# Performance work log

Measured on AMD Instinct MI355X. Metric: run time of the kernel, lower is better.

The kernel has to match this reference:

```python
import jax, jax.numpy as jnp
import numpy as np

B, S, D, H = 4, 2048, 1024, 16
DH = D // H


def setup_inputs() -> dict:
    key = jax.random.key(0)
    k1, k2, k3, k4, k5 = jax.random.split(key, 5)
    X = jax.random.normal(k1, (B, S, D), dtype=jnp.float32)
    W1 = jax.random.normal(k2, (3 * D, D), dtype=jnp.float32) * 0.02
    b1 = jax.random.normal(k3, (3 * D,), dtype=jnp.float32) * 0.01
    W2 = jax.random.normal(k4, (D, D), dtype=jnp.float32) * 0.02
    b2 = jax.random.normal(k5, (D,), dtype=jnp.float32) * 0.01
    return {"X": X, "W1": W1, "b1": b1, "W2": W2, "b2": b2}


def reference(X, W1, b1, W2, b2):
    b, s, d = X.shape
    # fused QKV projection (nn.Linear: y = x @ W.T + b)
    Y = X @ W1.T + b1                                   # [B,S,3D]
    Q, K, V = jnp.split(Y, 3, axis=2)                   # each [B,S,D]
    # reshape(x): view (B,S,H,DH) then permute(0,2,3,1) -> [B,H,DH,S]
    q = Q.reshape(b, s, H, DH).transpose(0, 2, 3, 1)    # [B,H,DH,S]
    v = V.reshape(b, s, H, DH).transpose(0, 2, 3, 1)    # [B,H,DH,S]
    # reshape(x, k=True): permute(0,2,1,3) -> [B,H,S,DH]
    k = K.reshape(b, s, H, DH).transpose(0, 2, 1, 3)    # [B,H,S,DH]
    # w = q @ k / sqrt(q.size(-1)) ; note q.size(-1) == S in this layout
    w = jnp.einsum('bhds,bhse->bhde', q, k) / jnp.sqrt(jnp.asarray(s, X.dtype))  # [B,H,DH,DH]
    w = jax.nn.softmax(w, axis=-1)
    out = jnp.einsum('bhde,bhes->bhds', w, v)           # [B,H,DH,S]
    # cat(): raw contiguous view of [B,H,DH,S] into [B,S,H*DH] (memory-order reshape)
    out = out.reshape(b, s, H * DH)                     # [B,S,D]
    return out @ W2.T + b2
```

## Files before the change

### kernel.cpp

```cpp
#include <hip/hip_runtime.h>
#include <stdint.h>

#define B_ 4
#define S_ 2048
#define D_ 1024
#define H_ 16
#define DH_ 64
#define M_TOT (B_*S_)
#define N1_ (3*D_)
#define K_ D_
#define NCH 8

typedef __bf16 bf16_8 __attribute__((ext_vector_type(8)));
typedef float  f32x4  __attribute__((ext_vector_type(4)));
typedef unsigned short u16;

typedef __attribute__((address_space(1))) const void* gas_t;
typedef __attribute__((address_space(3))) void*       las_t;

__device__ __forceinline__ unsigned short f2bf(float f) {
    union { float f; unsigned u; } v; v.f = f;
    unsigned r = v.u + 0x7FFFu + ((v.u >> 16) & 1u);
    return (unsigned short)(r >> 16);
}

__device__ __forceinline__ void async_ld16(const void* g, void* l) {
    __builtin_amdgcn_global_load_lds((gas_t)g, (las_t)l, 16, 0, 0);
}

__global__ __launch_bounds__(256)
void cast_kernel(const float* __restrict__ X, const float* __restrict__ W1,
                 const float* __restrict__ W2, unsigned short* __restrict__ Xb,
                 unsigned short* __restrict__ W1b, unsigned short* __restrict__ W2b) {
    const int nX  = (M_TOT * K_) / 4;
    const int nW1 = (N1_ * K_) / 4;
    int i = blockIdx.x * 256 + threadIdx.x;
    const float4* src; unsigned short* dst; int j;
    if (i < nX)            { src = (const float4*)X;  dst = Xb;  j = i; }
    else if (i < nX + nW1) { src = (const float4*)W1; dst = W1b; j = i - nX; }
    else                   { src = (const float4*)W2; dst = W2b; j = i - nX - nW1; }
    float4 v = src[j];
    ushort4 o;
    o.x = f2bf(v.x); o.y = f2bf(v.y); o.z = f2bf(v.z); o.w = f2bf(v.w);
    ((ushort4*)dst)[j] = o;
}

template<int N, int NBX, bool OUT_BF16>
__global__ __launch_bounds__(256)
void gemm_bt(const unsigned short* __restrict__ A,
             const unsigned short* __restrict__ Bm,
             const float* __restrict__ bias,
             void* __restrict__ C, int K) {
    __shared__ unsigned short As[128 * 64];
    __shared__ unsigned short Bs[128 * 64];
    const int t    = threadIdx.x;
    const int wid  = t >> 6;
    const int lane = t & 63;
    const int lrow = lane & 15;
    const int lq   = lane >> 4;

    const int lid  = blockIdx.y * NBX + blockIdx.x;
    const int xcd  = lid & 7;
    const int slot = lid >> 3;
    const int by   = xcd * (gridDim.y >> 3) + slot / NBX;
    const int bx   = slot % NBX;
    const int m0   = by * 128;
    const int n0   = bx * 128;

    const int wm   = (wid >> 1) * 64;
    const int wn   = (wid & 1) * 64;

    f32x4 acc[4][4] = {};

    for (int k0 = 0; k0 < K; k0 += 64) {
#pragma unroll
        for (int p = 0; p < 4; p++) {
            const int c   = p * 256 + t;
            const int row = c >> 3;
            const int kb  = (c & 7) ^ (row & 7);
            async_ld16(A  + (size_t)(m0 + row) * K + k0 + kb * 8, (char*)As + c * 16);
            async_ld16(Bm + (size_t)(n0 + row) * K + k0 + kb * 8, (char*)Bs + c * 16);
        }
        __syncthreads();

#pragma unroll
        for (int ks = 0; ks < 2; ks++) {
            bf16_8 af[4], bfr[4];
#pragma unroll
            for (int mt = 0; mt < 4; mt++) {
                const int r  = wm + mt * 16 + lrow;
                const int kb = (ks * 4 + lq) ^ (r & 7);
                af[mt] = *(const bf16_8*)(As + (r * 8 + kb) * 8);
            }
#pragma unroll
            for (int nt = 0; nt < 4; nt++) {
                const int r  = wn + nt * 16 + lrow;
                const int kb = (ks * 4 + lq) ^ (r & 7);
                bfr[nt] = *(const bf16_8*)(Bs + (r * 8 + kb) * 8);
            }
#pragma unroll
            for (int mt = 0; mt < 4; mt++)
#pragma unroll
                for (int nt = 0; nt < 4; nt++)
                    acc[mt][nt] = __builtin_amdgcn_mfma_f32_16x16x32_bf16(af[mt], bfr[nt], acc[mt][nt], 0, 0, 0);
        }
        __syncthreads();
    }

#pragma unroll
    for (int nt = 0; nt < 4; nt++) {
        const int col = n0 + wn + nt * 16 + lrow;
        const float bv = bias[col];
#pragma unroll
        for (int mt = 0; mt < 4; mt++) {
            const int row = m0 + wm + mt * 16 + lq * 4;
            f32x4 a = acc[mt][nt];
            if (OUT_BF16) {
                unsigned short* Cp = (unsigned short*)C;
#pragma unroll
                for (int i = 0; i < 4; i++)
                    Cp[(size_t)(row + i) * N + col] = f2bf(a[i] + bv);
            } else {
                float* Cp = (float*)C;
#pragma unroll
                for (int i = 0; i < 4; i++)
                    Cp[(size_t)(row + i) * N + col] = a[i] + bv;
            }
        }
    }
}

__global__ __launch_bounds__(256)
void attn_scores(const unsigned short* __restrict__ Y, float* __restrict__ Scp) {
    __shared__ unsigned short Qs[64 * 72];
    __shared__ unsigned short Ks[64 * 72];
    const int bh = blockIdx.x, ch = blockIdx.y;
    const int b = bh >> 4, h = bh & 15;
    const size_t ybase = (size_t)b * S_ * 3072;
    const int qoff = h * 64, koff = D_ + h * 64;
    const int t = threadIdx.x, wid = t >> 6, lane = t & 63;
    const int lrow = lane & 15, lq = lane >> 4;

    f32x4 acc[4] = {};
    const int sbeg = ch * (S_ / NCH);
    for (int s0 = sbeg; s0 < sbeg + S_ / NCH; s0 += 64) {
#pragma unroll
        for (int p = 0; p < 4; p++) {
            int idx = p * 256 + t;
            int r = idx >> 4, cg = (idx & 15) * 4;
            const size_t gb = ybase + (size_t)(s0 + r) * 3072;
            ushort4 q4 = *(const ushort4*)(Y + gb + qoff + cg);
            ushort4 k4 = *(const ushort4*)(Y + gb + koff + cg);
            Qs[(cg + 0) * 72 + r] = q4.x; Qs[(cg + 1) * 72 + r] = q4.y;
            Qs[(cg + 2) * 72 + r] = q4.z; Qs[(cg + 3) * 72 + r] = q4.w;
            Ks[(cg + 0) * 72 + r] = k4.x; Ks[(cg + 1) * 72 + r] = k4.y;
            Ks[(cg + 2) * 72 + r] = k4.z; Ks[(cg + 3) * 72 + r] = k4.w;
        }
        __syncthreads();
#pragma unroll
        for (int ks = 0; ks < 2; ks++) {
            bf16_8 aq = *(const bf16_8*)(Qs + (wid * 16 + lrow) * 72 + ks * 32 + lq * 8);
#pragma unroll
            for (int nt = 0; nt < 4; nt++) {
                bf16_8 bk = *(const bf16_8*)(Ks + (nt * 16 + lrow) * 72 + ks * 32 + lq * 8);
                acc[nt] = __builtin_amdgcn_mfma_f32_16x16x32_bf16(aq, bk, acc[nt], 0, 0, 0);
            }
        }
        __syncthreads();
    }

    float* out = Scp + (size_t)(bh * NCH + ch) * 64 * 64;
#pragma unroll
    for (int nt = 0; nt < 4; nt++)
#pragma unroll
        for (int i = 0; i < 4; i++)
            out[(wid * 16 + lq * 4 + i) * 64 + nt * 16 + lrow] = acc[nt][i];
}

__global__ __launch_bounds__(256)
void attn_out_fused(const unsigned short* __restrict__ Y,
                    const float* __restrict__ Scp,
                    unsigned short* __restrict__ O) {
    __shared__ unsigned short Ws[64 * 72];
    const int bh = blockIdx.x, sc = blockIdx.y;
    const int b = bh >> 4, h = bh & 15;
    const size_t ybase = (size_t)b * S_ * 3072;
    const int voff = 2 * D_ + h * 64;
    const int t = threadIdx.x, wid = t >> 6, lane = t & 63;
    const int lrow = lane & 15, lq = lane >> 4;

    {
        const int d = t >> 2, q = t & 3;
        float s[16] = {};
#pragma unroll
        for (int c = 0; c < NCH; c++) {
            const float4* p = (const float4*)(Scp + ((size_t)(bh * NCH + c) * 64 + d) * 64 + q * 16);
#pragma unroll
            for (int j = 0; j < 4; j++) {
                float4 v = p[j];
                s[j*4+0] += v.x; s[j*4+1] += v.y; s[j*4+2] += v.z; s[j*4+3] += v.w;
            }
        }
        const float scale = 0.022097086912079608f;
        float m = -3.0e38f;
#pragma unroll
        for (int i = 0; i < 16; i++) { s[i] *= scale; m = fmaxf(m, s[i]); }
        m = fmaxf(m, __shfl_xor(m, 1));
        m = fmaxf(m, __shfl_xor(m, 2));
        float sum = 0.f;
#pragma unroll
        for (int i = 0; i < 16; i++) { s[i] = __expf(s[i] - m); sum += s[i]; }
        sum += __shfl_xor(sum, 1);
        sum += __shfl_xor(sum, 2);
        const float inv = 1.0f / sum;
        unsigned short* w = Ws + d * 72 + q * 16;
#pragma unroll
        for (int i = 0; i < 16; i++) w[i] = f2bf(s[i] * inv);
    }
    __syncthreads();

    bf16_8 aw[4][2];
#pragma unroll
    for (int mt = 0; mt < 4; mt++)
#pragma unroll
        for (int ks = 0; ks < 2; ks++)
            aw[mt][ks] = *(const bf16_8*)(Ws + (mt * 16 + lrow) * 72 + ks * 32 + lq * 8);

    const size_t obase = (size_t)b * (H_ * DH_ * S_) + (size_t)h * (DH_ * S_);
    const int s0 = sc * 256 + wid * 64;
    f32x4 o[4][4] = {};
#pragma unroll
    for (int ks = 0; ks < 2; ks++) {
        bf16_8 bv[4];
#pragma unroll
        for (int nt = 0; nt < 4; nt++)
            bv[nt] = *(const bf16_8*)(Y + ybase + (size_t)(s0 + nt * 16 + lrow) * 3072 + voff + ks * 32 + lq * 8);
#pragma unroll
        for (int mt = 0; mt < 4; mt++)
#pragma unroll
            for (int nt = 0; nt < 4; nt++)
                o[mt][nt] = __builtin_amdgcn_mfma_f32_16x16x32_bf16(aw[mt][ks], bv[nt], o[mt][nt], 0, 0, 0);
    }
#pragma unroll
    for (int mt = 0; mt < 4; mt++)
#pragma unroll
        for (int nt = 0; nt < 4; nt++) {
            const int d = mt * 16 + lq * 4;
            const int s = s0 + nt * 16 + lrow;
#pragma unroll
            for (int i = 0; i < 4; i++)
                O[obase + (size_t)(d + i) * S_ + s] = f2bf(o[mt][nt][i]);
        }
}

extern "C" void kernel_launch(void* const* d_in, const int* in_sizes, int n_in,
                              void* d_out, int out_size, void* d_ws, size_t ws_size,
                              hipStream_t stream) {
    const float* X  = (const float*)d_in[0];
    const float* W1 = (const float*)d_in[1];
    const float* b1 = (const float*)d_in[2];
    const float* W2 = (const float*)d_in[3];
    const float* b2 = (const float*)d_in[4];

    char* ws = (char*)d_ws;
    unsigned short* Xb  = (unsigned short*)(ws + 0);
    unsigned short* W1b = (unsigned short*)(ws + (16u << 20));
    unsigned short* W2b = (unsigned short*)(ws + (22u << 20));
    unsigned short* Yb  = (unsigned short*)(ws + (24u << 20));
    unsigned short* Ob  = (unsigned short*)(ws + (1u << 20));
    float* Scp = (float*)d_out;

    cast_kernel<<<12288, 256, 0, stream>>>(X, W1, W2, Xb, W1b, W2b);
    gemm_bt<N1_, N1_/128, true><<<dim3(N1_ / 128, M_TOT / 128), 256, 0, stream>>>(Xb, W1b, b1, Yb, K_);
    attn_scores<<<dim3(64, NCH), 256, 0, stream>>>(Yb, Scp);
    attn_out_fused<<<dim3(64, NCH), 256, 0, stream>>>(Yb, Scp, Ob);
    gemm_bt<D_, D_/128, false><<<dim3(D_ / 128, M_TOT / 128), 256, 0, stream>>>(Ob, W2b, b2, d_out, K_);
}
```

Measured before the change: 210.6 us.

## Write Q/K transposed from QKV GEMM epilogue, drop LDS transpose in scores

The QKV GEMM epilogue now scatters Q and K into per-head [B,H,DH,S] transposed buffers, written as ushort4 along S, and V into a separate [B,S,D] buffer. The score kernel then loads MFMA operands straight from global memory with no shared-memory transpose and no barriers. This removes the LDS staging and syncs in attn_scores and shrinks V row stride for the output kernel. In exchange, the V stores in the GEMM epilogue become four strided scalar stores, and the scores kernel depends on global-load latency with no LDS reuse.

```diff
diff --git a/kernel.cpp b/kernel.cpp
--- a/kernel.cpp
+++ b/kernel.cpp
@@ -45,12 +45,13 @@
     ((ushort4*)dst)[j] = o;
 }
 
-template<int N, int NBX, bool OUT_BF16>
+template<int N, int NBX, int EPI>
 __global__ __launch_bounds__(256)
 void gemm_bt(const unsigned short* __restrict__ A,
              const unsigned short* __restrict__ Bm,
              const float* __restrict__ bias,
-             void* __restrict__ C, int K) {
+             void* __restrict__ C, int K,
+             u16* __restrict__ QT, u16* __restrict__ KT, u16* __restrict__ Vb) {
     __shared__ unsigned short As[128 * 64];
     __shared__ unsigned short Bs[128 * 64];
     const int t    = threadIdx.x;
@@ -115,11 +116,23 @@
         for (int mt = 0; mt < 4; mt++) {
             const int row = m0 + wm + mt * 16 + lq * 4;
             f32x4 a = acc[mt][nt];
-            if (OUT_BF16) {
-                unsigned short* Cp = (unsigned short*)C;
-#pragma unroll
-                for (int i = 0; i < 4; i++)
-                    Cp[(size_t)(row + i) * N + col] = f2bf(a[i] + bv);
+            if constexpr (EPI == 2) {
+                ushort4 o;
+                o.x = f2bf(a[0] + bv); o.y = f2bf(a[1] + bv);
+                o.z = f2bf(a[2] + bv); o.w = f2bf(a[3] + bv);
+                const int b = row >> 11, s = row & 2047;
+                const int d = col & 63;
+                if (col < 1024) {
+                    *(ushort4*)(QT + ((size_t)(b * 16 + (col >> 6)) * 64 + d) * (size_t)S_ + s) = o;
+                } else if (col < 2048) {
+                    *(ushort4*)(KT + ((size_t)(b * 16 + ((col >> 6) - 16)) * 64 + d) * (size_t)S_ + s) = o;
+                } else {
+                    u16* vp = Vb + ((size_t)b * S_ + s) * (size_t)D_ + (col - 2048);
+                    vp[0]      = o.x;
+                    vp[D_]     = o.y;
+                    vp[2 * D_] = o.z;
+                    vp[3 * D_] = o.w;
+                }
             } else {
                 float* Cp = (float*)C;
 #pragma unroll
@@ -131,42 +144,29 @@
 }
 
 __global__ __launch_bounds__(256)
-void attn_scores(const unsigned short* __restrict__ Y, float* __restrict__ Scp) {
-    __shared__ unsigned short Qs[64 * 72];
-    __shared__ unsigned short Ks[64 * 72];
+void attn_scores_t(const u16* __restrict__ QT, const u16* __restrict__ KT,
+                   float* __restrict__ Scp) {
     const int bh = blockIdx.x, ch = blockIdx.y;
-    const int b = bh >> 4, h = bh & 15;
-    const size_t ybase = (size_t)b * S_ * 3072;
-    const int qoff = h * 64, koff = D_ + h * 64;
     const int t = threadIdx.x, wid = t >> 6, lane = t & 63;
     const int lrow = lane & 15, lq = lane >> 4;
 
+    const u16* Qh = QT + (size_t)bh * 64 * S_;
+    const u16* Kh = KT + (size_t)bh * 64 * S_;
+
     f32x4 acc[4] = {};
     const int sbeg = ch * (S_ / NCH);
-    for (int s0 = sbeg; s0 < sbeg + S_ / NCH; s0 += 64) {
-#pragma unroll
-        for (int p = 0; p < 4; p++) {
-            int idx = p * 256 + t;
-            int r = idx >> 4, cg = (idx & 15) * 4;
-            const size_t gb = ybase + (size_t)(s0 + r) * 3072;
-            ushort4 q4 = *(const ushort4*)(Y + gb + qoff + cg);
-            ushort4 k4 = *(const ushort4*)(Y + gb + koff + cg);
-            Qs[(cg + 0) * 72 + r] = q4.x; Qs[(cg + 1) * 72 + r] = q4.y;
-            Qs[(cg + 2) * 72 + r] = q4.z; Qs[(cg + 3) * 72 + r] = q4.w;
-            Ks[(cg + 0) * 72 + r] = k4.x; Ks[(cg + 1) * 72 + r] = k4.y;
-            Ks[(cg + 2) * 72 + r] = k4.z; Ks[(cg + 3) * 72 + r] = k4.w;
-        }
-        __syncthreads();
-#pragma unroll
-        for (int ks = 0; ks < 2; ks++) {
-            bf16_8 aq = *(const bf16_8*)(Qs + (wid * 16 + lrow) * 72 + ks * 32 + lq * 8);
-#pragma unroll
-            for (int nt = 0; nt < 4; nt++) {
-                bf16_8 bk = *(const bf16_8*)(Ks + (nt * 16 + lrow) * 72 + ks * 32 + lq * 8);
-                acc[nt] = __builtin_amdgcn_mfma_f32_16x16x32_bf16(aq, bk, acc[nt], 0, 0, 0);
-            }
-        }
-        __syncthreads();
+#pragma unroll 2
+    for (int s0 = sbeg; s0 < sbeg + S_ / NCH; s0 += 32) {
+        const int so = s0 + lq * 8;
+        bf16_8 aq = *(const bf16_8*)(Qh + (wid * 16 + lrow) * S_ + so);
+        bf16_8 bk0 = *(const bf16_8*)(Kh + ( 0 + lrow) * S_ + so);
+        bf16_8 bk1 = *(const bf16_8*)(Kh + (16 + lrow) * S_ + so);
+        bf16_8 bk2 = *(const bf16_8*)(Kh + (32 + lrow) * S_ + so);
+        bf16_8 bk3 = *(const bf16_8*)(Kh + (48 + lrow) * S_ + so);
+        acc[0] = __builtin_amdgcn_mfma_f32_16x16x32_bf16(aq, bk0, acc[0], 0, 0, 0);
+        acc[1] = __builtin_amdgcn_mfma_f32_16x16x32_bf16(aq, bk1, acc[1], 0, 0, 0);
+        acc[2] = __builtin_amdgcn_mfma_f32_16x16x32_bf16(aq, bk2, acc[2], 0, 0, 0);
+        acc[3] = __builtin_amdgcn_mfma_f32_16x16x32_bf16(aq, bk3, acc[3], 0, 0, 0);
     }
 
     float* out = Scp + (size_t)(bh * NCH + ch) * 64 * 64;
@@ -178,14 +178,14 @@
 }
 
 __global__ __launch_bounds__(256)
-void attn_out_fused(const unsigned short* __restrict__ Y,
+void attn_out_fused(const unsigned short* __restrict__ Vb,
                     const float* __restrict__ Scp,
                     unsigned short* __restrict__ O) {
     __shared__ unsigned short Ws[64 * 72];
     const int bh = blockIdx.x, sc = blockIdx.y;
     const int b = bh >> 4, h = bh & 15;
-    const size_t ybase = (size_t)b * S_ * 3072;
-    const int voff = 2 * D_ + h * 64;
+    const size_t vbase = (size_t)b * S_ * D_;
+    const int voff = h * 64;
     const int t = threadIdx.x, wid = t >> 6, lane = t & 63;
     const int lrow = lane & 15, lq = lane >> 4;
 
@@ -234,7 +234,7 @@
         bf16_8 bv[4];
 #pragma unroll
         for (int nt = 0; nt < 4; nt++)
-            bv[nt] = *(const bf16_8*)(Y + ybase + (size_t)(s0 + nt * 16 + lrow) * 3072 + voff + ks * 32 + lq * 8);
+            bv[nt] = *(const bf16_8*)(Vb + vbase + (size_t)(s0 + nt * 16 + lrow) * D_ + voff + ks * 32 + lq * 8);
 #pragma unroll
         for (int mt = 0; mt < 4; mt++)
 #pragma unroll
@@ -266,13 +266,17 @@
     unsigned short* Xb  = (unsigned short*)(ws + 0);
     unsigned short* W1b = (unsigned short*)(ws + (16u << 20));
     unsigned short* W2b = (unsigned short*)(ws + (22u << 20));
-    unsigned short* Yb  = (unsigned short*)(ws + (24u << 20));
+    unsigned short* QT  = (unsigned short*)(ws + (24u << 20));
+    unsigned short* KT  = (unsigned short*)(ws + (40u << 20));
+    unsigned short* Vb  = (unsigned short*)(ws + (56u << 20));
     unsigned short* Ob  = (unsigned short*)(ws + (1u << 20));
     float* Scp = (float*)d_out;
 
     cast_kernel<<<12288, 256, 0, stream>>>(X, W1, W2, Xb, W1b, W2b);
-    gemm_bt<N1_, N1_/128, true><<<dim3(N1_ / 128, M_TOT / 128), 256, 0, stream>>>(Xb, W1b, b1, Yb, K_);
-    attn_scores<<<dim3(64, NCH), 256, 0, stream>>>(Yb, Scp);
-    attn_out_fused<<<dim3(64, NCH), 256, 0, stream>>>(Yb, Scp, Ob);
-    gemm_bt<D_, D_/128, false><<<dim3(D_ / 128, M_TOT / 128), 256, 0, stream>>>(Ob, W2b, b2, d_out, K_);
-}
+    gemm_bt<N1_, N1_/128, 2><<<dim3(N1_ / 128, M_TOT / 128), 256, 0, stream>>>(
+        Xb, W1b, b1, nullptr, K_, QT, KT, Vb);
+    attn_scores_t<<<dim3(64, NCH), 256, 0, stream>>>(QT, KT, Scp);
+    attn_out_fused<<<dim3(64, NCH), 256, 0, stream>>>(Vb, Scp, Ob);
+    gemm_bt<D_, D_/128, 0><<<dim3(D_ / 128, M_TOT / 128), 256, 0, stream>>>(
+        Ob, W2b, b2, d_out, K_, nullptr, nullptr, nullptr);
+}
```

Result: no change. 213.8 us (+1.5%).
